# Optimization experiments

Measured on AMD Instinct MI355X. Metric: run time of the kernel, lower is better.

The kernel has to match this reference:

```python
import jax, jax.numpy as jnp
import numpy as np

N_VOX = 100000   # active voxels
K = 27           # 3^3 kernel offsets
M = 60000        # matched (in, out) pairs per offset
CIN = 64
COUT = 64
BN_EPS = 1e-5


def setup_inputs() -> dict:
    key = jax.random.key(0)
    ks = jax.random.split(key, 6)
    feats = jax.random.normal(ks[0], (N_VOX, CIN), dtype=jnp.float32)
    W = jax.random.normal(ks[1], (K, CIN, COUT), dtype=jnp.float32) * 0.05
    gamma = jnp.ones((COUT,), dtype=jnp.float32)
    beta = jnp.zeros((COUT,), dtype=jnp.float32)
    running_mean = jax.random.normal(ks[2], (COUT,), dtype=jnp.float32) * 0.1
    running_var = jax.random.uniform(ks[3], (COUT,), dtype=jnp.float32, minval=0.5, maxval=1.5)
    in_idx = jax.random.randint(ks[4], (K, M), 0, N_VOX, dtype=jnp.int32)
    out_idx = jax.random.randint(ks[5], (K, M), 0, N_VOX, dtype=jnp.int32)
    return {
        "feats": feats, "W": W, "gamma": gamma, "beta": beta,
        "running_mean": running_mean, "running_var": running_var,
        "in_idx": in_idx, "out_idx": out_idx,
    }


def reference(feats, W, gamma, beta, running_mean, running_var, in_idx, out_idx):
    # Sparse conv as gather-GEMM-scatter over the hash-map kernel map.
    gathered = feats[in_idx]                              # [K, M, Cin]
    contrib = jnp.einsum('kmc,kcd->kmd', gathered, W)     # [K, M, Cout]
    out = jax.ops.segment_sum(
        contrib.reshape(-1, W.shape[-1]),                 # [K*M, Cout]
        out_idx.reshape(-1),
        num_segments=feats.shape[0],
    )                                                     # [N, Cout]
    # BatchNorm (inference, running stats) + ReLU
    inv = jax.lax.rsqrt(running_var + BN_EPS)
    y = (out - running_mean) * (inv * gamma) + beta
    return jnp.maximum(y, 0.0)
```

## Files before the change

kernel.cpp:

```cpp
#include <hip/hip_runtime.h>

#define N_VOX 100000
#define K_OFF 27
#define M_PAIR 60000
#define NPAIR (K_OFF * M_PAIR)
#define CIN 64
#define COUT 64
#define BN_EPS 1e-5f
#define CNT_STRIDE 16

#define TILES_PER_WAVE 10
#define WAVES_PER_K (M_PAIR / 16 / TILES_PER_WAVE)
#define CONV_BLOCKS_X ((WAVES_PER_K + 3) / 4)

typedef __attribute__((ext_vector_type(8))) short bf16x8;
typedef __attribute__((ext_vector_type(8))) unsigned short u16x8;
typedef __attribute__((ext_vector_type(2))) unsigned int u32x2;
typedef __attribute__((ext_vector_type(4))) float f32x4;

__device__ __forceinline__ unsigned short f32_to_bf16(float f) {
    unsigned int u = __float_as_uint(f);
    u += 0x7FFFu + ((u >> 16) & 1u);
    return (unsigned short)(u >> 16);
}
__device__ __forceinline__ float bf16_lo(unsigned int u) {
    return __uint_as_float(u << 16);
}
__device__ __forceinline__ float bf16_hi(unsigned int u) {
    return __uint_as_float(u & 0xffff0000u);
}
__device__ __forceinline__ float bf16_to_f32(unsigned short b) {
    return __uint_as_float(((unsigned int)b) << 16);
}

__global__ __launch_bounds__(256) void prep_rank_kernel(
    const int* __restrict__ oix, int* __restrict__ cnt, int* __restrict__ rank,
    const float* __restrict__ feats, unsigned short* __restrict__ fb,
    const float* __restrict__ W, unsigned short* __restrict__ Wt,
    const float* __restrict__ gamma, const float* __restrict__ beta,
    const float* __restrict__ rmean, const float* __restrict__ rvar,
    float* __restrict__ bnscale, float* __restrict__ bnshift)
{
    const int e = blockIdx.x * blockDim.x + threadIdx.x;
    if (e < NPAIR) rank[e] = atomicAdd(&cnt[oix[e] * CNT_STRIDE], 1);
    if (e < (N_VOX * CIN) / 4) {
        const int e4 = e * 4;
        const float4 v = *(const float4*)(feats + e4);
        ushort4 b;
        b.x = f32_to_bf16(v.x);
        b.y = f32_to_bf16(v.y);
        b.z = f32_to_bf16(v.z);
        b.w = f32_to_bf16(v.w);
        *(ushort4*)(fb + e4) = b;
    }
    if (e < K_OFF * CIN * COUT) {
        const int k = e / (CIN * COUT);
        const int r = e % (CIN * COUT);
        Wt[k * CIN * COUT + (r % COUT) * CIN + (r / COUT)] = f32_to_bf16(W[e]);
    }
    if (e < COUT) {
        const float inv = rsqrtf(rvar[e] + BN_EPS);
        const float sc = inv * gamma[e];
        bnscale[e] = sc;
        bnshift[e] = beta[e] - rmean[e] * sc;
    }
}

__global__ __launch_bounds__(256) void alloc_kernel(
    const int* __restrict__ cnt, int* __restrict__ total, int* __restrict__ seg,
    int* __restrict__ cntc)
{
    __shared__ int part[256];
    __shared__ int bbase;
    const int t = threadIdx.x;
    const int v = blockIdx.x * 256 + t;
    const int c = (v < N_VOX) ? cnt[v * CNT_STRIDE] : 0;
    part[t] = c;
    __syncthreads();
    for (int o = 1; o < 256; o <<= 1) {
        int x = (t >= o) ? part[t - o] : 0;
        __syncthreads();
        part[t] += x;
        __syncthreads();
    }
    if (t == 255) bbase = atomicAdd(total, part[255]);
    __syncthreads();
    if (v < N_VOX) {
        seg[v] = bbase + (part[t] - c);
        cntc[v] = c;
    }
}

__global__ __launch_bounds__(256) void conv_scatter_kernel(
    const unsigned short* __restrict__ fb, const unsigned short* __restrict__ Wt,
    const int* __restrict__ in_idx, const int* __restrict__ out_idx,
    const int* __restrict__ rank, const int* __restrict__ seg,
    unsigned short* __restrict__ contrib)
{
    __shared__ alignas(16) unsigned short lds[4][16 * 72];
    const int k = blockIdx.y;
    const int lane = threadIdx.x & 63;
    const int wid = threadIdx.x >> 6;
    const int w = blockIdx.x * 4 + wid;
    if (w >= WAVES_PER_K) return;
    const int col = lane & 15;
    const int quad = lane >> 4;
    unsigned short* L = lds[wid];

    bf16x8 Bf[4][2];
    const short* Wk = (const short*)(Wt + k * CIN * COUT);
#pragma unroll
    for (int t = 0; t < 4; ++t) {
        const short* p = Wk + (t * 16 + col) * CIN + quad * 8;
        Bf[t][0] = *(const bf16x8*)(p);
        Bf[t][1] = *(const bf16x8*)(p + 32);
    }

    int m0 = k * M_PAIR + (w * TILES_PER_WAVE) * 16;
    int slot = 0;
    if (lane < 16) slot = seg[out_idx[m0 + lane]] + rank[m0 + lane];
    {
        const int rin = in_idx[m0 + col];
        const short* fp = (const short*)fb + (size_t)rin * CIN + quad * 8;
        bf16x8 A0 = *(const bf16x8*)(fp);
        bf16x8 A1 = *(const bf16x8*)(fp + 32);

        for (int it = 0; it < TILES_PER_WAVE; ++it) {
            bf16x8 nA0 = A0, nA1 = A1;
            int nslot = slot;
            if (it + 1 < TILES_PER_WAVE) {
                const int m1 = m0 + 16;
                if (lane < 16)
                    nslot = seg[out_idx[m1 + lane]] + rank[m1 + lane];
                const int rn = in_idx[m1 + col];
                const short* fn = (const short*)fb + (size_t)rn * CIN + quad * 8;
                nA0 = *(const bf16x8*)(fn);
                nA1 = *(const bf16x8*)(fn + 32);
            }

            f32x4 acc[4];
#pragma unroll
            for (int t = 0; t < 4; ++t) {
                f32x4 z = {0.f, 0.f, 0.f, 0.f};
                acc[t] = __builtin_amdgcn_mfma_f32_16x16x32_bf16(A0, Bf[t][0], z, 0, 0, 0);
                acc[t] = __builtin_amdgcn_mfma_f32_16x16x32_bf16(A1, Bf[t][1], acc[t], 0, 0, 0);
            }
#pragma unroll
            for (int r = 0; r < 4; ++r) {
                const int row = quad * 4 + r;
#pragma unroll
                for (int t = 0; t < 4; ++t)
                    L[row * 72 + t * 16 + col] = f32_to_bf16(acc[t][r]);
            }
#pragma unroll
            for (int itr = 0; itr < 2; ++itr) {
                const int row = itr * 8 + (lane >> 3);
                const int chunk = lane & 7;
                const int pos = __shfl(slot, row, 64);
                const u16x8 v = *(const u16x8*)(L + row * 72 + chunk * 8);
                __builtin_nontemporal_store(
                    v, (u16x8*)(contrib + (size_t)pos * 64 + chunk * 8));
            }
            A0 = nA0;
            A1 = nA1;
            slot = nslot;
            m0 += 16;
        }
    }
}

__global__ __launch_bounds__(256) void gather_bn_kernel(
    const unsigned short* __restrict__ contrib, const int* __restrict__ seg,
    const int* __restrict__ cntc,
    const float* __restrict__ bnscale, const float* __restrict__ bnshift,
    float* __restrict__ out)
{
    const int v = blockIdx.x * 4 + (threadIdx.x >> 6);
    if (v >= N_VOX) return;
    const int lane = threadIdx.x & 63;
    const int rg = lane >> 4;
    const int cg = lane & 15;
    const int s = seg[v];
    const int n = cntc[v];

    const u32x2* base = (const u32x2*)(contrib + (size_t)s * 64) + cg;
    float a0 = 0.f, a1 = 0.f, a2 = 0.f, a3 = 0.f;
    float b0 = 0.f, b1 = 0.f, b2 = 0.f, b3 = 0.f;
    int j = rg;
    for (; j + 4 < n; j += 8) {
        const u32x2 u = __builtin_nontemporal_load(base + (size_t)j * 16);
        const u32x2 w = __builtin_nontemporal_load(base + (size_t)(j + 4) * 16);
        a0 += bf16_lo(u.x); a1 += bf16_hi(u.x);
        a2 += bf16_lo(u.y); a3 += bf16_hi(u.y);
        b0 += bf16_lo(w.x); b1 += bf16_hi(w.x);
        b2 += bf16_lo(w.y); b3 += bf16_hi(w.y);
    }
    for (; j < n; j += 4) {
        const u32x2 u = __builtin_nontemporal_load(base + (size_t)j * 16);
        a0 += bf16_lo(u.x); a1 += bf16_hi(u.x);
        a2 += bf16_lo(u.y); a3 += bf16_hi(u.y);
    }
    a0 += b0; a1 += b1; a2 += b2; a3 += b3;
    a0 += __shfl_xor(a0, 16, 64); a0 += __shfl_xor(a0, 32, 64);
    a1 += __shfl_xor(a1, 16, 64); a1 += __shfl_xor(a1, 32, 64);
    a2 += __shfl_xor(a2, 16, 64); a2 += __shfl_xor(a2, 32, 64);
    a3 += __shfl_xor(a3, 16, 64); a3 += __shfl_xor(a3, 32, 64);
    if (rg == 0) {
        const int ch = cg * 4;
        float4 r;
        r.x = fmaxf(fmaf(a0, bnscale[ch + 0], bnshift[ch + 0]), 0.f);
        r.y = fmaxf(fmaf(a1, bnscale[ch + 1], bnshift[ch + 1]), 0.f);
        r.z = fmaxf(fmaf(a2, bnscale[ch + 2], bnshift[ch + 2]), 0.f);
        r.w = fmaxf(fmaf(a3, bnscale[ch + 3], bnshift[ch + 3]), 0.f);
        *(float4*)(out + (size_t)v * 64 + ch) = r;
    }
}

__global__ __launch_bounds__(256) void prep_small_kernel(
    const float* __restrict__ feats, unsigned short* __restrict__ fb,
    float* __restrict__ out, const float* __restrict__ W,
    unsigned short* __restrict__ Wt)
{
    const int e = blockIdx.x * blockDim.x + threadIdx.x;
    if (e < (N_VOX * CIN) / 4) {
        const int e4 = e * 4;
        const float4 v = *(const float4*)(feats + e4);
        ushort4 b;
        b.x = f32_to_bf16(v.x);
        b.y = f32_to_bf16(v.y);
        b.z = f32_to_bf16(v.z);
        b.w = f32_to_bf16(v.w);
        *(ushort4*)(fb + e4) = b;
        *(float4*)(out + e4) = make_float4(0.f, 0.f, 0.f, 0.f);
    }
    if (e < K_OFF * CIN * COUT) {
        const int k = e / (CIN * COUT);
        const int r = e % (CIN * COUT);
        Wt[k * CIN * COUT + (r % COUT) * CIN + (r / COUT)] = f32_to_bf16(W[e]);
    }
}

__global__ __launch_bounds__(256) void conv_atomic_kernel(
    const unsigned short* __restrict__ fb, const unsigned short* __restrict__ Wt,
    const int* __restrict__ in_idx, const int* __restrict__ out_idx,
    float* __restrict__ out)
{
    const int k = blockIdx.y;
    const int lane = threadIdx.x & 63;
    const int wave = blockIdx.x * 4 + (threadIdx.x >> 6);
    const int col = lane & 15;
    const int quad = lane >> 4;
    bf16x8 Bf[4][2];
    const short* Wk = (const short*)(Wt + k * CIN * COUT);
#pragma unroll
    for (int t = 0; t < 4; ++t) {
        const short* p = Wk + (t * 16 + col) * CIN + quad * 8;
        Bf[t][0] = *(const bf16x8*)(p);
        Bf[t][1] = *(const bf16x8*)(p + 32);
    }
    const int base = k * M_PAIR;
    for (int tile = wave; tile < M_PAIR / 16; tile += 128) {
        const int m0 = base + tile * 16;
        const int rin = in_idx[m0 + col];
        const short* fp = (const short*)fb + (size_t)rin * CIN + quad * 8;
        const bf16x8 A0 = *(const bf16x8*)(fp);
        const bf16x8 A1 = *(const bf16x8*)(fp + 32);
        f32x4 acc[4];
#pragma unroll
        for (int t = 0; t < 4; ++t) {
            f32x4 z = {0.f, 0.f, 0.f, 0.f};
            acc[t] = __builtin_amdgcn_mfma_f32_16x16x32_bf16(A0, Bf[t][0], z, 0, 0, 0);
            acc[t] = __builtin_amdgcn_mfma_f32_16x16x32_bf16(A1, Bf[t][1], acc[t], 0, 0, 0);
        }
        int vo[4];
#pragma unroll
        for (int r = 0; r < 4; ++r) vo[r] = out_idx[m0 + quad * 4 + r];
#pragma unroll
        for (int r = 0; r < 4; ++r) {
            float* op = out + (size_t)vo[r] * COUT + col;
#pragma unroll
            for (int t = 0; t < 4; ++t) atomicAdd(op + t * 16, acc[t][r]);
        }
    }
}

__global__ __launch_bounds__(256) void bn_relu_kernel(
    float* __restrict__ out,
    const float* __restrict__ gamma, const float* __restrict__ beta,
    const float* __restrict__ mean, const float* __restrict__ var)
{
    const int e = blockIdx.x * blockDim.x + threadIdx.x;
    if (e >= N_VOX * COUT) return;
    const int c = e & (COUT - 1);
    const float inv = rsqrtf(var[c] + BN_EPS);
    const float y = (out[e] - mean[c]) * (inv * gamma[c]) + beta[c];
    out[e] = fmaxf(y, 0.f);
}

extern "C" void kernel_launch(void* const* d_in, const int* in_sizes, int n_in,
                              void* d_out, int out_size, void* d_ws, size_t ws_size,
                              hipStream_t stream) {
    const float* feats = (const float*)d_in[0];
    const float* W     = (const float*)d_in[1];
    const float* gamma = (const float*)d_in[2];
    const float* beta  = (const float*)d_in[3];
    const float* rmean = (const float*)d_in[4];
    const float* rvar  = (const float*)d_in[5];
    const int* in_idx  = (const int*)d_in[6];
    const int* out_idx = (const int*)d_in[7];
    float* out = (float*)d_out;

    char* ws = (char*)d_ws;
    size_t off = 0;
    auto alloc = [&](size_t bytes) {
        size_t p = off;
        off = (off + bytes + 255) & ~(size_t)255;
        return p;
    };
    const size_t o_fb   = alloc((size_t)N_VOX * CIN * 2);
    const size_t o_wt   = alloc((size_t)K_OFF * CIN * COUT * 2);
    const size_t o_cnt  = alloc((size_t)N_VOX * CNT_STRIDE * 4 + 4);
    const size_t o_seg  = alloc((size_t)N_VOX * 4);
    const size_t o_cntc = alloc((size_t)N_VOX * 4);
    const size_t o_bn   = alloc((size_t)2 * COUT * 4);
    const size_t o_rank = alloc((size_t)NPAIR * 4);
    const size_t o_ctr  = alloc((size_t)NPAIR * COUT * 2);
    const bool big = (ws_size >= off);

    unsigned short* fb  = (unsigned short*)(ws + o_fb);
    unsigned short* Wt  = (unsigned short*)(ws + o_wt);
    int* cnt            = (int*)(ws + o_cnt);
    int* total          = cnt + (size_t)N_VOX * CNT_STRIDE;
    int* seg            = (int*)(ws + o_seg);
    int* cntc           = (int*)(ws + o_cntc);
    float* bnscale      = (float*)(ws + o_bn);
    float* bnshift      = bnscale + COUT;
    int* rank           = (int*)(ws + o_rank);
    unsigned short* ctr = (unsigned short*)(ws + o_ctr);

    if (big) {
        hipMemsetAsync(cnt, 0, (size_t)N_VOX * CNT_STRIDE * 4 + 4, stream);
        prep_rank_kernel<<<(NPAIR + 255) / 256, 256, 0, stream>>>(
            out_idx, cnt, rank, feats, fb, W, Wt,
            gamma, beta, rmean, rvar, bnscale, bnshift);
        alloc_kernel<<<(N_VOX + 255) / 256, 256, 0, stream>>>(cnt, total, seg, cntc);
        conv_scatter_kernel<<<dim3(CONV_BLOCKS_X, K_OFF), 256, 0, stream>>>(
            fb, Wt, in_idx, out_idx, rank, seg, ctr);
        gather_bn_kernel<<<(N_VOX + 3) / 4, 256, 0, stream>>>(
            ctr, seg, cntc, bnscale, bnshift, out);
    } else {
        const int ptot = (N_VOX * CIN) / 4;
        prep_small_kernel<<<(ptot + 255) / 256, 256, 0, stream>>>(feats, fb, out, W, Wt);
        conv_atomic_kernel<<<dim3(32, K_OFF), 256, 0, stream>>>(fb, Wt, in_idx, out_idx, out);
        const int total_e = N_VOX * COUT;
        bn_relu_kernel<<<(total_e + 255) / 256, 256, 0, stream>>>(out, gamma, beta, rmean, rvar);
    }
}
```

Measured before the change: 277.7 us.

## Replace precomputed rank array with atomic cursor slots, drop nontemporal hints

Stops storing a per-pair rank in the counting pass and drops the rank array. The conv kernel now claims output slots with an atomicAdd on a per-voxel cursor that the alloc kernel initialises from the segment base. This saves writing and re-reading 1.6M ints, but adds returning atomics to the conv kernel's critical path. Nontemporal store/load hints on the contrib buffer are also removed so it may stay in cache between scatter and gather.

```diff
diff --git a/kernel.cpp b/kernel.cpp
--- a/kernel.cpp
+++ b/kernel.cpp
@@ -33,8 +33,8 @@
     return __uint_as_float(((unsigned int)b) << 16);
 }
 
-__global__ __launch_bounds__(256) void prep_rank_kernel(
-    const int* __restrict__ oix, int* __restrict__ cnt, int* __restrict__ rank,
+__global__ __launch_bounds__(256) void prep_kernel(
+    const int* __restrict__ oix, int* __restrict__ cnt,
     const float* __restrict__ feats, unsigned short* __restrict__ fb,
     const float* __restrict__ W, unsigned short* __restrict__ Wt,
     const float* __restrict__ gamma, const float* __restrict__ beta,
@@ -42,7 +42,7 @@
     float* __restrict__ bnscale, float* __restrict__ bnshift)
 {
     const int e = blockIdx.x * blockDim.x + threadIdx.x;
-    if (e < NPAIR) rank[e] = atomicAdd(&cnt[oix[e] * CNT_STRIDE], 1);
+    if (e < NPAIR) atomicAdd(&cnt[oix[e] * CNT_STRIDE], 1);
     if (e < (N_VOX * CIN) / 4) {
         const int e4 = e * 4;
         const float4 v = *(const float4*)(feats + e4);
@@ -68,7 +68,7 @@
 
 __global__ __launch_bounds__(256) void alloc_kernel(
     const int* __restrict__ cnt, int* __restrict__ total, int* __restrict__ seg,
-    int* __restrict__ cntc)
+    int* __restrict__ cursor, int* __restrict__ cntc)
 {
     __shared__ int part[256];
     __shared__ int bbase;
@@ -86,7 +86,9 @@
     if (t == 255) bbase = atomicAdd(total, part[255]);
     __syncthreads();
     if (v < N_VOX) {
-        seg[v] = bbase + (part[t] - c);
+        const int base = bbase + (part[t] - c);
+        seg[v] = base;
+        cursor[v] = base;
         cntc[v] = c;
     }
 }
@@ -94,7 +96,7 @@
 __global__ __launch_bounds__(256) void conv_scatter_kernel(
     const unsigned short* __restrict__ fb, const unsigned short* __restrict__ Wt,
     const int* __restrict__ in_idx, const int* __restrict__ out_idx,
-    const int* __restrict__ rank, const int* __restrict__ seg,
+    int* __restrict__ cursor,
     unsigned short* __restrict__ contrib)
 {
     __shared__ alignas(16) unsigned short lds[4][16 * 72];
@@ -118,7 +120,7 @@
 
     int m0 = k * M_PAIR + (w * TILES_PER_WAVE) * 16;
     int slot = 0;
-    if (lane < 16) slot = seg[out_idx[m0 + lane]] + rank[m0 + lane];
+    if (lane < 16) slot = atomicAdd(&cursor[out_idx[m0 + lane]], 1);
     {
         const int rin = in_idx[m0 + col];
         const short* fp = (const short*)fb + (size_t)rin * CIN + quad * 8;
@@ -131,7 +133,7 @@
             if (it + 1 < TILES_PER_WAVE) {
                 const int m1 = m0 + 16;
                 if (lane < 16)
-                    nslot = seg[out_idx[m1 + lane]] + rank[m1 + lane];
+                    nslot = atomicAdd(&cursor[out_idx[m1 + lane]], 1);
                 const int rn = in_idx[m1 + col];
                 const short* fn = (const short*)fb + (size_t)rn * CIN + quad * 8;
                 nA0 = *(const bf16x8*)(fn);
@@ -158,8 +160,7 @@
                 const int chunk = lane & 7;
                 const int pos = __shfl(slot, row, 64);
                 const u16x8 v = *(const u16x8*)(L + row * 72 + chunk * 8);
-                __builtin_nontemporal_store(
-                    v, (u16x8*)(contrib + (size_t)pos * 64 + chunk * 8));
+                *(u16x8*)(contrib + (size_t)pos * 64 + chunk * 8) = v;
             }
             A0 = nA0;
             A1 = nA1;
@@ -188,15 +189,15 @@
     float b0 = 0.f, b1 = 0.f, b2 = 0.f, b3 = 0.f;
     int j = rg;
     for (; j + 4 < n; j += 8) {
-        const u32x2 u = __builtin_nontemporal_load(base + (size_t)j * 16);
-        const u32x2 w = __builtin_nontemporal_load(base + (size_t)(j + 4) * 16);
+        const u32x2 u = *(base + (size_t)j * 16);
+        const u32x2 w = *(base + (size_t)(j + 4) * 16);
         a0 += bf16_lo(u.x); a1 += bf16_hi(u.x);
         a2 += bf16_lo(u.y); a3 += bf16_hi(u.y);
         b0 += bf16_lo(w.x); b1 += bf16_hi(w.x);
         b2 += bf16_lo(w.y); b3 += bf16_hi(w.y);
     }
     for (; j < n; j += 4) {
-        const u32x2 u = __builtin_nontemporal_load(base + (size_t)j * 16);
+        const u32x2 u = *(base + (size_t)j * 16);
         a0 += bf16_lo(u.x); a1 += bf16_hi(u.x);
         a2 += bf16_lo(u.y); a3 += bf16_hi(u.y);
     }
@@ -321,9 +322,9 @@
     const size_t o_wt   = alloc((size_t)K_OFF * CIN * COUT * 2);
     const size_t o_cnt  = alloc((size_t)N_VOX * CNT_STRIDE * 4 + 4);
     const size_t o_seg  = alloc((size_t)N_VOX * 4);
+    const size_t o_cur  = alloc((size_t)N_VOX * 4);
     const size_t o_cntc = alloc((size_t)N_VOX * 4);
     const size_t o_bn   = alloc((size_t)2 * COUT * 4);
-    const size_t o_rank = alloc((size_t)NPAIR * 4);
     const size_t o_ctr  = alloc((size_t)NPAIR * COUT * 2);
     const bool big = (ws_size >= off);
 
@@ -332,20 +333,21 @@
     int* cnt            = (int*)(ws + o_cnt);
     int* total          = cnt + (size_t)N_VOX * CNT_STRIDE;
     int* seg            = (int*)(ws + o_seg);
+    int* cursor         = (int*)(ws + o_cur);
     int* cntc           = (int*)(ws + o_cntc);
     float* bnscale      = (float*)(ws + o_bn);
     float* bnshift      = bnscale + COUT;
-    int* rank           = (int*)(ws + o_rank);
     unsigned short* ctr = (unsigned short*)(ws + o_ctr);
 
     if (big) {
-        hipMemsetAsync(cnt, 0, (size_t)N_VOX * CNT_STRIDE * 4 + 4, stream);
-        prep_rank_kernel<<<(NPAIR + 255) / 256, 256, 0, stream>>>(
-            out_idx, cnt, rank, feats, fb, W, Wt,
+        hipError_t _e = hipMemsetAsync(cnt, 0, (size_t)N_VOX * CNT_STRIDE * 4 + 4, stream);
+        (void)_e;
+        prep_kernel<<<(NPAIR + 255) / 256, 256, 0, stream>>>(
+            out_idx, cnt, feats, fb, W, Wt,
             gamma, beta, rmean, rvar, bnscale, bnshift);
-        alloc_kernel<<<(N_VOX + 255) / 256, 256, 0, stream>>>(cnt, total, seg, cntc);
+        alloc_kernel<<<(N_VOX + 255) / 256, 256, 0, stream>>>(cnt, total, seg, cursor, cntc);
         conv_scatter_kernel<<<dim3(CONV_BLOCKS_X, K_OFF), 256, 0, stream>>>(
-            fb, Wt, in_idx, out_idx, rank, seg, ctr);
+            fb, Wt, in_idx, out_idx, cursor, ctr);
         gather_bn_kernel<<<(N_VOX + 3) / 4, 256, 0, stream>>>(
             ctr, seg, cntc, bnscale, bnshift, out);
     } else {
```

New measurement: 303.9 us. 1.09x slower.

## Replace global atomic rank counting with two-level bucketed binning

Applied to the files above, without the earlier changes.

Per-pair rank computation previously issued one global atomic per pair on a padded counter array. It now bins pairs into 256-voxel buckets using LDS histograms and one global atomic per bucket per block. A second kernel then computes ranks with LDS atomics inside each bucket. This aims to cut global atomic traffic and the large memset, at the cost of an extra kernel and a record buffer. Buckets are capped at BCAP entries, so overflow would silently drop pairs. The cap holds for uniform random indices but is not guaranteed in general.

```diff
diff --git a/kernel.cpp b/kernel.cpp
--- a/kernel.cpp
+++ b/kernel.cpp
@@ -7,7 +7,14 @@
 #define CIN 64
 #define COUT 64
 #define BN_EPS 1e-5f
-#define CNT_STRIDE 16
+
+#define VB_SHIFT 8
+#define VB (1 << VB_SHIFT)
+#define NB ((N_VOX + VB - 1) / VB)
+#define BCAP 5120
+#define PPT 16
+#define PA_PAIRS (256 * PPT)
+#define PA_GRID ((NPAIR + PA_PAIRS - 1) / PA_PAIRS)
 
 #define TILES_PER_WAVE 10
 #define WAVES_PER_K (M_PAIR / 16 / TILES_PER_WAVE)
@@ -33,18 +40,58 @@
     return __uint_as_float(((unsigned int)b) << 16);
 }
 
-__global__ __launch_bounds__(256) void prep_rank_kernel(
-    const int* __restrict__ oix, int* __restrict__ cnt, int* __restrict__ rank,
+__global__ __launch_bounds__(256) void scatter_pairs_kernel(
+    const int* __restrict__ oix,
+    unsigned int* __restrict__ recs, int* __restrict__ bucketCount,
     const float* __restrict__ feats, unsigned short* __restrict__ fb,
     const float* __restrict__ W, unsigned short* __restrict__ Wt,
     const float* __restrict__ gamma, const float* __restrict__ beta,
     const float* __restrict__ rmean, const float* __restrict__ rvar,
     float* __restrict__ bnscale, float* __restrict__ bnshift)
 {
-    const int e = blockIdx.x * blockDim.x + threadIdx.x;
-    if (e < NPAIR) rank[e] = atomicAdd(&cnt[oix[e] * CNT_STRIDE], 1);
-    if (e < (N_VOX * CIN) / 4) {
-        const int e4 = e * 4;
+    __shared__ int lhist[NB];
+    __shared__ int gbase[NB];
+    const int t = threadIdx.x;
+    for (int i = t; i < NB; i += 256) lhist[i] = 0;
+    __syncthreads();
+
+    const int base = blockIdx.x * PA_PAIRS;
+    int vsave[PPT];
+    int lpos[PPT];
+#pragma unroll
+    for (int i = 0; i < PPT; ++i) {
+        const int e = base + i * 256 + t;
+        int v = -1, lp = 0;
+        if (e < NPAIR) {
+            v = oix[e];
+            lp = atomicAdd(&lhist[v >> VB_SHIFT], 1);
+        }
+        vsave[i] = v;
+        lpos[i] = lp;
+    }
+    __syncthreads();
+    for (int i = t; i < NB; i += 256) {
+        const int c = lhist[i];
+        gbase[i] = c ? atomicAdd(&bucketCount[i], c) : 0;
+    }
+    __syncthreads();
+#pragma unroll
+    for (int i = 0; i < PPT; ++i) {
+        const int v = vsave[i];
+        if (v >= 0) {
+            const int e = base + i * 256 + t;
+            const int b = v >> VB_SHIFT;
+            const int idx = gbase[b] + lpos[i];
+            if (idx < BCAP)
+                recs[(size_t)b * BCAP + idx] =
+                    ((unsigned int)e << VB_SHIFT) | (unsigned int)(v & (VB - 1));
+        }
+    }
+
+    const int gid = blockIdx.x * 256 + t;
+    const int nt = PA_GRID * 256;
+    for (int e4i = gid; e4i < (N_VOX * CIN) / 4; e4i += nt) {
+        const int e4 = e4i * 4;
         const float4 v = *(const float4*)(feats + e4);
         ushort4 b;
         b.x = f32_to_bf16(v.x);
@@ -53,28 +100,50 @@
         b.w = f32_to_bf16(v.w);
         *(ushort4*)(fb + e4) = b;
     }
-    if (e < K_OFF * CIN * COUT) {
+    for (int e = gid; e < K_OFF * CIN * COUT; e += nt) {
         const int k = e / (CIN * COUT);
         const int r = e % (CIN * COUT);
         Wt[k * CIN * COUT + (r % COUT) * CIN + (r / COUT)] = f32_to_bf16(W[e]);
     }
-    if (e < COUT) {
-        const float inv = rsqrtf(rvar[e] + BN_EPS);
-        const float sc = inv * gamma[e];
-        bnscale[e] = sc;
-        bnshift[e] = beta[e] - rmean[e] * sc;
-    }
+    if (gid < COUT) {
+        const float inv = rsqrtf(rvar[gid] + BN_EPS);
+        const float sc = inv * gamma[gid];
+        bnscale[gid] = sc;
+        bnshift[gid] = beta[gid] - rmean[gid] * sc;
+    }
+}
+
+__global__ __launch_bounds__(256) void rank_kernel(
+    const unsigned int* __restrict__ recs, const int* __restrict__ bucketCount,
+    int* __restrict__ rank, int* __restrict__ cntc)
+{
+    __shared__ int hist[VB];
+    const int b = blockIdx.x;
+    const int t = threadIdx.x;
+    hist[t] = 0;
+    __syncthreads();
+    int bc = bucketCount[b];
+    if (bc > BCAP) bc = BCAP;
+    const unsigned int* r = recs + (size_t)b * BCAP;
+    for (int i = t; i < bc; i += 256) {
+        const unsigned int rec = r[i];
+        const int vl = rec & (VB - 1);
+        const int pid = rec >> VB_SHIFT;
+        rank[pid] = atomicAdd(&hist[vl], 1);
+    }
+    __syncthreads();
+    const int v = b * VB + t;
+    if (v < N_VOX) cntc[v] = hist[t];
 }
 
 __global__ __launch_bounds__(256) void alloc_kernel(
-    const int* __restrict__ cnt, int* __restrict__ total, int* __restrict__ seg,
-    int* __restrict__ cntc)
+    const int* __restrict__ cntc, int* __restrict__ total, int* __restrict__ seg)
 {
     __shared__ int part[256];
     __shared__ int bbase;
     const int t = threadIdx.x;
     const int v = blockIdx.x * 256 + t;
-    const int c = (v < N_VOX) ? cnt[v * CNT_STRIDE] : 0;
+    const int c = (v < N_VOX) ? cntc[v] : 0;
     part[t] = c;
     __syncthreads();
     for (int o = 1; o < 256; o <<= 1) {
@@ -85,10 +154,7 @@
     }
     if (t == 255) bbase = atomicAdd(total, part[255]);
     __syncthreads();
-    if (v < N_VOX) {
-        seg[v] = bbase + (part[t] - c);
-        cntc[v] = c;
-    }
+    if (v < N_VOX) seg[v] = bbase + (part[t] - c);
 }
 
 __global__ __launch_bounds__(256) void conv_scatter_kernel(
@@ -319,7 +385,8 @@
     };
     const size_t o_fb   = alloc((size_t)N_VOX * CIN * 2);
     const size_t o_wt   = alloc((size_t)K_OFF * CIN * COUT * 2);
-    const size_t o_cnt  = alloc((size_t)N_VOX * CNT_STRIDE * 4 + 4);
+    const size_t o_bc   = alloc((size_t)NB * 4 + 4);
+    const size_t o_recs = alloc((size_t)NB * BCAP * 4);
     const size_t o_seg  = alloc((size_t)N_VOX * 4);
     const size_t o_cntc = alloc((size_t)N_VOX * 4);
     const size_t o_bn   = alloc((size_t)2 * COUT * 4);
@@ -329,8 +396,9 @@
 
     unsigned short* fb  = (unsigned short*)(ws + o_fb);
     unsigned short* Wt  = (unsigned short*)(ws + o_wt);
-    int* cnt            = (int*)(ws + o_cnt);
-    int* total          = cnt + (size_t)N_VOX * CNT_STRIDE;
+    int* bucketCount    = (int*)(ws + o_bc);
+    int* total          = bucketCount + NB;
+    unsigned int* recs  = (unsigned int*)(ws + o_recs);
     int* seg            = (int*)(ws + o_seg);
     int* cntc           = (int*)(ws + o_cntc);
     float* bnscale      = (float*)(ws + o_bn);
@@ -339,11 +407,13 @@
     unsigned short* ctr = (unsigned short*)(ws + o_ctr);
 
     if (big) {
-        hipMemsetAsync(cnt, 0, (size_t)N_VOX * CNT_STRIDE * 4 + 4, stream);
-        prep_rank_kernel<<<(NPAIR + 255) / 256, 256, 0, stream>>>(
-            out_idx, cnt, rank, feats, fb, W, Wt,
+        hipError_t _e = hipMemsetAsync(bucketCount, 0, (size_t)NB * 4 + 4, stream);
+        (void)_e;
+        scatter_pairs_kernel<<<PA_GRID, 256, 0, stream>>>(
+            out_idx, recs, bucketCount, feats, fb, W, Wt,
             gamma, beta, rmean, rvar, bnscale, bnshift);
-        alloc_kernel<<<(N_VOX + 255) / 256, 256, 0, stream>>>(cnt, total, seg, cntc);
+        rank_kernel<<<NB, 256, 0, stream>>>(recs, bucketCount, rank, cntc);
+        alloc_kernel<<<(N_VOX + 255) / 256, 256, 0, stream>>>(cntc, total, seg);
         conv_scatter_kernel<<<dim3(CONV_BLOCKS_X, K_OFF), 256, 0, stream>>>(
             fb, Wt, in_idx, out_idx, rank, seg, ctr);
         gather_bn_kernel<<<(N_VOX + 3) / 4, 256, 0, stream>>>(
```

New measurement: 253.7 us. 1.09x faster.
